# Kernel tuning notes

Measured on AMD Instinct MI355X. Metric: run time of the kernel, lower is better.

## Reference

```python
import jax, jax.numpy as jnp
import numpy as np

E = 128      # emb_size
VD = 128     # v_dim
NH = 4       # num_heads
WX = 7       # window_sizex
WY = 7       # window_sizey
B, HH, WW_ = 16, 112, 112


def setup_inputs() -> dict:
    key = jax.random.key(0)
    k0, k1, k2, k3 = jax.random.split(key, 4)
    return {
        "x": jax.random.normal(k0, (B, HH, WW_, E), jnp.float32),
        "v": jax.random.normal(k1, (B, HH, WW_, VD), jnp.float32),
        "Wqk": jax.random.normal(k2, (2 * E, E), jnp.float32) * 0.02,
        "bqk": jnp.zeros((2 * E,), jnp.float32),
        "pos_emb": jax.random.normal(k3, (2 * WX - 1, 2 * WY - 1), jnp.float32),
    }


def reference(x, v, Wqk, bqk, pos_emb):
    b, h, w, _ = x.shape
    e, ev = E // NH, VD // NH
    s = WX * WY
    Wh, Ww = h // WX, w // WY

    # qk projection: [b,h,w,2E] -> split as (c k) with c=E, k=2
    qk = (x @ Wqk.T + bqk).reshape(b, h, w, E, 2)

    # shifted roll: note original uses -window//2 = -4 (python floor div)
    qk = jnp.roll(qk, ((-WX) // 2, (-WY) // 2), axis=(1, 2))
    v = jnp.roll(v, ((-WX) // 2, (-WY) // 2), axis=(1, 2))

    # window partition; channel split is (e H): e outer, head inner
    qk = qk.reshape(b, Wh, WX, Ww, WY, e, NH, 2)
    qk = qk.transpose(0, 6, 1, 3, 2, 4, 5, 7).reshape(b, NH, Wh, Ww, s, e, 2)
    q, k_ = qk[..., 0], qk[..., 1]
    vw = v.reshape(b, Wh, WX, Ww, WY, ev, NH)
    vw = vw.transpose(0, 6, 1, 3, 2, 4, 5).reshape(b, NH, Wh, Ww, s, ev)

    scores = jnp.einsum('bhxyse,bhxyte->bhxyst', q, k_) / np.float32(np.sqrt(E / NH))

    # relative position bias lookup
    idx = np.indices((WX, WY)).transpose(1, 2, 0).reshape(s, 2)
    rel = idx[None, :, :] - idx[:, None, :] + np.array([WX - 1, WY - 1])
    scores = scores + pos_emb[rel[..., 0], rel[..., 1]]

    # shift masks (added to last window-row and last window-column)
    m = WX * (WY // 2)  # 21
    row_mask = np.zeros((s, s), np.float32)
    row_mask[-m:, :-m] = -np.inf
    row_mask[:-m, -m:] = -np.inf
    col_mask = row_mask.reshape(s // WX, WX, s // WY, WY).transpose(1, 0, 3, 2).reshape(s, s)
    scores = scores.at[:, :, -1, :].add(jnp.asarray(row_mask))
    scores = scores.at[:, :, :, -1].add(jnp.asarray(col_mask))

    attn = jax.nn.softmax(scores, axis=-1)
    out = jnp.einsum('bhxyst,bhxyte->bhxyse', attn, vw)

    # merge windows back: b H Wh Ww (w1 w2) e -> b (Wh w1) (Ww w2) (e H)
    out = out.reshape(b, NH, Wh, Ww, WX, WY, ev)
    out = out.transpose(0, 2, 4, 3, 5, 6, 1).reshape(b, h, w, VD)

    # un-roll: original uses +window//2 = +3 (asymmetric w.r.t. the -4 roll, kept faithful)
    out = jnp.roll(out, (WX // 2, WY // 2), axis=(1, 2))
    return out
```

## Files before the change

### kernel.cpp

```cpp
#include <hip/hip_runtime.h>
#include <hip/hip_bf16.h>
#include <math.h>

#define NH_ 4
#define S_  49
#define B_  16
#define H_  112
#define W_  112
#define WT  16

typedef __attribute__((ext_vector_type(8))) short short8;
typedef __attribute__((ext_vector_type(4))) float f32x4;

__device__ __forceinline__ unsigned short f2bf(float f) {
  union { __hip_bfloat16 h; unsigned short u; } c;
  c.h = __float2bfloat16(f);
  return c.u;
}
__device__ __forceinline__ short8 cvt8(float4 a, float4 b) {
  union { short8 s; unsigned short u[8]; } r;
  r.u[0] = f2bf(a.x); r.u[1] = f2bf(a.y); r.u[2] = f2bf(a.z); r.u[3] = f2bf(a.w);
  r.u[4] = f2bf(b.x); r.u[5] = f2bf(b.y); r.u[6] = f2bf(b.z); r.u[7] = f2bf(b.w);
  return r.s;
}

__global__ void wprep(const float* __restrict__ Wqk, unsigned short* __restrict__ Wb) {
  int oi = (blockIdx.x * 256 + threadIdx.x) * 4;
  int np = oi >> 7;
  int k  = oi & 127;
  int h = np >> 6, c = np & 63;
  int orig = 8 * (c >> 1) + 2 * h + (c & 1);
  float4 w = *(const float4*)(Wqk + orig * 128 + k);
  ushort4 o; o.x = f2bf(w.x); o.y = f2bf(w.y); o.z = f2bf(w.z); o.w = f2bf(w.w);
  *(ushort4*)(Wb + oi) = o;
}

#define PSTR   4112
#define SM_VT  32896
#define SM_POS 51328
#define SM_TOT 52004

__global__ __launch_bounds__(256, 3) void swin_fused(
    const float* __restrict__ x, const float* __restrict__ v,
    const float* __restrict__ bqk, const float* __restrict__ pos,
    const unsigned short* __restrict__ Wb, float* __restrict__ out)
{
  __shared__ __align__(16) char smem[SM_TOT];
  float* posl = (float*)(smem + SM_POS);

  const int tid  = threadIdx.x;
  const int lane = tid & 63;
  const int g    = lane >> 4, l15 = lane & 15;
  const int wv   = tid >> 6;
  const int blk  = blockIdx.x;
  const int ww   = blk % WT, wh = (blk / WT) % WT, b = blk / (WT * WT);

  if (tid < 169) posl[tid] = pos[tid];

  float bq[4];
  #pragma unroll
  for (int q = 0; q < 4; ++q)
    bq[q] = bqk[64 * q + 8 * (l15 >> 1) + 2 * wv + (l15 & 1)];

  float4 vS[8];
  #pragma unroll
  for (int it = 0; it < 2; ++it) {
    const int idx = tid + it * 256;
    const int e = idx & 31, p4 = idx >> 5;
    #pragma unroll
    for (int j = 0; j < 4; ++j) {
      const int p = p4 * 4 + j;
      float4 vv = {0.f, 0.f, 0.f, 0.f};
      if (p < S_) {
        const int px = p / 7, py = p % 7;
        const int gi = (wh * 7 + px + 4) % H_;
        const int gj = (ww * 7 + py + 4) % W_;
        vv = ((const float4*)(v + (((size_t)b * H_ + gi) * W_ + gj) * 128))[e];
      }
      vS[it * 4 + j] = vv;
    }
  }

  short8 af[4][4];
  #pragma unroll
  for (int mt = 0; mt < 4; ++mt) {
    const int prow = 16 * mt + l15;
    const int pc = prow < S_ ? prow : S_ - 1;
    const int px = pc / 7, py = pc % 7;
    const int gi = (wh * 7 + px + 4) % H_;
    const int gj = (ww * 7 + py + 4) % W_;
    const float* xrow = x + (((size_t)b * H_ + gi) * W_ + gj) * 128;
    #pragma unroll
    for (int kk = 0; kk < 4; ++kk) {
      float4 a0 = *(const float4*)(xrow + kk * 32 + g * 8);
      float4 a1 = *(const float4*)(xrow + kk * 32 + g * 8 + 4);
      af[mt][kk] = cvt8(a0, a1);
    }
  }

  #pragma unroll
  for (int it = 0; it < 2; ++it) {
    const int idx = tid + it * 256;
    const int e = idx & 31, p4 = idx >> 5;
    const int kbase = 32 * (p4 >> 3) + 8 * (p4 & 3) + 4 * ((p4 >> 2) & 1);
    union { ushort4 v4; unsigned short u[4]; } hv[4];
    #pragma unroll
    for (int j = 0; j < 4; ++j) {
      float4 vv = vS[it * 4 + j];
      hv[0].u[j] = f2bf(vv.x); hv[1].u[j] = f2bf(vv.y);
      hv[2].u[j] = f2bf(vv.z); hv[3].u[j] = f2bf(vv.w);
    }
    #pragma unroll
    for (int h = 0; h < 4; ++h)
      *(ushort4*)(smem + SM_VT + h * 4608 + e * 144 + kbase * 2) = hv[h].v4;
  }

  {
    char* plane0 = smem + (wv * 2) * PSTR;
    #pragma unroll
    for (int q = 0; q < 4; ++q) {
      const int nb = (wv * 64 + q * 16 + l15) * 128;
      short8 bfr[4];
      #pragma unroll
      for (int kk = 0; kk < 4; ++kk)
        bfr[kk] = *(const short8*)(Wb + nb + kk * 32 + g * 8);
      const float bias = bq[q];
      char* plane = plane0 + (l15 & 1) * PSTR;
      const int eoff = (q * 8 + (l15 >> 1)) * 2;
      #pragma unroll
      for (int mt = 0; mt < 4; ++mt) {
        f32x4 acc = {0.f, 0.f, 0.f, 0.f};
        #pragma unroll
        for (int kk = 0; kk < 4; ++kk)
          acc = __builtin_amdgcn_mfma_f32_16x16x32_bf16(af[mt][kk], bfr[kk], acc, 0, 0, 0);
        const int mbase = 16 * mt + 4 * g;
        #pragma unroll
        for (int r = 0; r < 4; ++r)
          *(unsigned short*)(plane + (mbase + r) * 64 + eoff) = f2bf(acc[r] + bias);
      }
    }
  }

  const bool maskR = (wh == WT - 1), maskC = (ww == WT - 1);
  const char* qpl = smem + (wv * 2 + 0) * PSTR;
  const char* kpl = smem + (wv * 2 + 1) * PSTR;
  short8 qf[4], kf[4];
  #pragma unroll
  for (int t4 = 0; t4 < 4; ++t4) {
    qf[t4] = *(const short8*)(qpl + (16 * t4 + l15) * 64 + g * 16);
    kf[t4] = *(const short8*)(kpl + (16 * t4 + l15) * 64 + g * 16);
  }

  f32x4 st[4][4];
  #pragma unroll
  for (int nt = 0; nt < 4; ++nt)
    #pragma unroll
    for (int mt = 0; mt < 4; ++mt) {
      f32x4 z = {0.f, 0.f, 0.f, 0.f};
      st[nt][mt] = __builtin_amdgcn_mfma_f32_16x16x32_bf16(kf[nt], qf[mt], z, 0, 0, 0);
    }

  int tix[4][4]; bool txg[4][4], tyg[4][4], tvl[4][4];
  #pragma unroll
  for (int nt = 0; nt < 4; ++nt)
    #pragma unroll
    for (int r = 0; r < 4; ++r) {
      const int t = 16 * nt + 4 * g + r;
      const int tx = t / 7, ty = t - 7 * tx;
      tix[nt][r] = tx * 13 + ty;
      txg[nt][r] = (tx >= 4); tyg[nt][r] = (ty >= 4);
      tvl[nt][r] = (t < S_);
    }

  if (maskR || maskC) {
    #pragma unroll
    for (int mt = 0; mt < 4; ++mt) {
      const int m = 16 * mt + l15;
      const int mc = m < S_ ? m : S_ - 1;
      const int px = mc / 7, py = mc - 7 * px;
      const bool pxg = (px >= 4), pyg = (py >= 4);
      #pragma unroll
      for (int nt = 0; nt < 4; ++nt)
        #pragma unroll
        for (int r = 0; r < 4; ++r) {
          if ((maskR && (pxg != txg[nt][r])) || (maskC && (pyg != tyg[nt][r])))
            st[nt][mt][r] = -INFINITY;
        }
    }
  }

  __syncthreads();

  const float scale = 0.17677669529663687f;
  short8 pvb[4][2];
  #pragma unroll
  for (int mt = 0; mt < 4; ++mt) {
    const int m = 16 * mt + l15;
    const int mc = m < S_ ? m : S_ - 1;
    const int px = mc / 7, py = mc - 7 * px;
    const int pofs = 84 - px * 13 - py;
    union { short8 s8; unsigned short h[8]; } pk[2];
    #pragma unroll
    for (int nt = 0; nt < 4; ++nt)
      #pragma unroll
      for (int r = 0; r < 4; ++r) {
        float s = st[nt][mt][r] * scale + posl[tix[nt][r] + pofs];
        float e = tvl[nt][r] ? __expf(s) : 0.f;
        pk[nt >> 1].h[(nt & 1) * 4 + r] = f2bf(e);
      }
    pvb[mt][0] = pk[0].s8;
    pvb[mt][1] = pk[1].s8;
  }

  f32x4 o_[2][4], d_[4];
  #pragma unroll
  for (int mt = 0; mt < 4; ++mt) {
    o_[0][mt] = (f32x4){0.f, 0.f, 0.f, 0.f};
    o_[1][mt] = (f32x4){0.f, 0.f, 0.f, 0.f};
    d_[mt]    = (f32x4){0.f, 0.f, 0.f, 0.f};
  }
  {
    const char* Vb = smem + SM_VT + wv * 4608;
    union { short8 s8; unsigned short h[8]; } one;
    #pragma unroll
    for (int j = 0; j < 8; ++j) one.h[j] = 0x3F80;
    #pragma unroll
    for (int ks = 0; ks < 2; ++ks) {
      short8 va[2];
      #pragma unroll
      for (int et = 0; et < 2; ++et)
        va[et] = *(const short8*)(Vb + (16 * et + l15) * 144 + ks * 64 + g * 16);
      #pragma unroll
      for (int mt = 0; mt < 4; ++mt) {
        o_[0][mt] = __builtin_amdgcn_mfma_f32_16x16x32_bf16(va[0], pvb[mt][ks], o_[0][mt], 0, 0, 0);
        o_[1][mt] = __builtin_amdgcn_mfma_f32_16x16x32_bf16(va[1], pvb[mt][ks], o_[1][mt], 0, 0, 0);
        d_[mt]    = __builtin_amdgcn_mfma_f32_16x16x32_bf16(one.s8, pvb[mt][ks], d_[mt], 0, 0, 0);
      }
    }
  }

  float (*outb)[132] = (float (*)[132])smem;
  #pragma unroll
  for (int mt = 0; mt < 4; ++mt) {
    const int m = 16 * mt + l15;
    if (m < S_) {
      const float inv = 1.f / d_[mt][0];
      #pragma unroll
      for (int et = 0; et < 2; ++et)
        #pragma unroll
        for (int r = 0; r < 4; ++r)
          outb[m][(16 * et + 4 * g + r) * 4 + wv] = o_[et][mt][r] * inv;
    }
  }
  __syncthreads();

  for (int idx = tid; idx < S_ * 32; idx += 256) {
    const int pp = idx >> 5, c4 = idx & 31;
    const int ppx = pp / 7, ppy = pp % 7;
    const int fi = (wh * 7 + ppx + 3) % H_;
    const int fj = (ww * 7 + ppy + 3) % W_;
    float4 val = *(const float4*)&outb[pp][c4 * 4];
    ((float4*)(out + (((size_t)b * H_ + fi) * W_ + fj) * 128))[c4] = val;
  }
}

extern "C" void kernel_launch(void* const* d_in, const int* in_sizes, int n_in,
                              void* d_out, int out_size, void* d_ws, size_t ws_size,
                              hipStream_t stream) {
  const float* x   = (const float*)d_in[0];
  const float* v   = (const float*)d_in[1];
  const float* Wqk = (const float*)d_in[2];
  const float* bqk = (const float*)d_in[3];
  const float* pos = (const float*)d_in[4];
  float* out = (float*)d_out;
  unsigned short* Wb = (unsigned short*)d_ws;

  hipLaunchKernelGGL(wprep, dim3(32), dim3(256), 0, stream, Wqk, Wb);
  hipLaunchKernelGGL(swin_fused, dim3(B_ * WT * WT), dim3(256), 0, stream,
                     x, v, bqk, pos, Wb, out);
}
```

Before: 110.5 us.

## Load V directly into MFMA register fragments, drop LDS staging, raise occupancy

V values are now gathered per lane straight from global memory as scalar floats, converted to bf16, and packed into MFMA B-operand fragments in registers. This removes the transposed LDS staging buffer for V and its stores and loads. Shared memory use drops from about 52KB to 33.5KB, and launch bounds go from 3 to 4 blocks per SM for more occupancy. In exchange, global loads become scalar and strided (one float per lane per element) instead of float4 and coalesced, and register pressure rises under the tighter launch bound.

```diff
diff --git a/kernel.cpp b/kernel.cpp
--- a/kernel.cpp
+++ b/kernel.cpp
@@ -36,11 +36,10 @@
 }
 
 #define PSTR   4112
-#define SM_VT  32896
-#define SM_POS 51328
-#define SM_TOT 52004
-
-__global__ __launch_bounds__(256, 3) void swin_fused(
+#define SM_POS 32896
+#define SM_TOT 33572
+
+__global__ __launch_bounds__(256, 4) void swin_fused(
     const float* __restrict__ x, const float* __restrict__ v,
     const float* __restrict__ bqk, const float* __restrict__ pos,
     const unsigned short* __restrict__ Wb, float* __restrict__ out)
@@ -62,23 +61,36 @@
   for (int q = 0; q < 4; ++q)
     bq[q] = bqk[64 * q + 8 * (l15 >> 1) + 2 * wv + (l15 & 1)];
 
-  float4 vS[8];
-  #pragma unroll
-  for (int it = 0; it < 2; ++it) {
-    const int idx = tid + it * 256;
-    const int e = idx & 31, p4 = idx >> 5;
-    #pragma unroll
-    for (int j = 0; j < 4; ++j) {
-      const int p = p4 * 4 + j;
-      float4 vv = {0.f, 0.f, 0.f, 0.f};
-      if (p < S_) {
-        const int px = p / 7, py = p % 7;
+  short8 vfr[2][2];
+  {
+    int voff[16]; bool vok[16];
+    #pragma unroll
+    for (int u = 0; u < 4; ++u)
+      #pragma unroll
+      for (int jr = 0; jr < 4; ++jr) {
+        const int t = 16 * u + 4 * g + jr;
+        const bool ok = (t < S_);
+        const int tc = ok ? t : 0;
+        const int px = tc / 7, py = tc - 7 * px;
         const int gi = (wh * 7 + px + 4) % H_;
         const int gj = (ww * 7 + py + 4) % W_;
-        vv = ((const float4*)(v + (((size_t)b * H_ + gi) * W_ + gj) * 128))[e];
-      }
-      vS[it * 4 + j] = vv;
-    }
+        voff[u * 4 + jr] = (gi * W_ + gj) * 128 + 4 * l15 + wv;
+        vok[u * 4 + jr] = ok;
+      }
+    const float* vb_ = v + (size_t)b * H_ * W_ * 128;
+    #pragma unroll
+    for (int et = 0; et < 2; ++et)
+      #pragma unroll
+      for (int ks = 0; ks < 2; ++ks) {
+        union { short8 s8; unsigned short h[8]; } pku;
+        #pragma unroll
+        for (int j = 0; j < 8; ++j) {
+          const int i16 = (2 * ks + (j >> 2)) * 4 + (j & 3);
+          float val = vok[i16] ? vb_[voff[i16] + et * 64] : 0.f;
+          pku.h[j] = f2bf(val);
+        }
+        vfr[et][ks] = pku.s8;
+      }
   }
 
   short8 af[4][4];
@@ -98,23 +110,6 @@
     }
   }
 
-  #pragma unroll
-  for (int it = 0; it < 2; ++it) {
-    const int idx = tid + it * 256;
-    const int e = idx & 31, p4 = idx >> 5;
-    const int kbase = 32 * (p4 >> 3) + 8 * (p4 & 3) + 4 * ((p4 >> 2) & 1);
-    union { ushort4 v4; unsigned short u[4]; } hv[4];
-    #pragma unroll
-    for (int j = 0; j < 4; ++j) {
-      float4 vv = vS[it * 4 + j];
-      hv[0].u[j] = f2bf(vv.x); hv[1].u[j] = f2bf(vv.y);
-      hv[2].u[j] = f2bf(vv.z); hv[3].u[j] = f2bf(vv.w);
-    }
-    #pragma unroll
-    for (int h = 0; h < 4; ++h)
-      *(ushort4*)(smem + SM_VT + h * 4608 + e * 144 + kbase * 2) = hv[h].v4;
-  }
-
   {
     char* plane0 = smem + (wv * 2) * PSTR;
     #pragma unroll
@@ -220,21 +215,16 @@
     d_[mt]    = (f32x4){0.f, 0.f, 0.f, 0.f};
   }
   {
-    const char* Vb = smem + SM_VT + wv * 4608;
     union { short8 s8; unsigned short h[8]; } one;
     #pragma unroll
     for (int j = 0; j < 8; ++j) one.h[j] = 0x3F80;
     #pragma unroll
     for (int ks = 0; ks < 2; ++ks) {
-      short8 va[2];
-      #pragma unroll
-      for (int et = 0; et < 2; ++et)
-        va[et] = *(const short8*)(Vb + (16 * et + l15) * 144 + ks * 64 + g * 16);
       #pragma unroll
       for (int mt = 0; mt < 4; ++mt) {
-        o_[0][mt] = __builtin_amdgcn_mfma_f32_16x16x32_bf16(va[0], pvb[mt][ks], o_[0][mt], 0, 0, 0);
-        o_[1][mt] = __builtin_amdgcn_mfma_f32_16x16x32_bf16(va[1], pvb[mt][ks], o_[1][mt], 0, 0, 0);
-        d_[mt]    = __builtin_amdgcn_mfma_f32_16x16x32_bf16(one.s8, pvb[mt][ks], d_[mt], 0, 0, 0);
+        o_[0][mt] = __builtin_amdgcn_mfma_f32_16x16x32_bf16(vfr[0][ks], pvb[mt][ks], o_[0][mt], 0, 0, 0);
+        o_[1][mt] = __builtin_amdgcn_mfma_f32_16x16x32_bf16(vfr[1][ks], pvb[mt][ks], o_[1][mt], 0, 0, 0);
+        d_[mt]    = __builtin_amdgcn_mfma_f32_16x16x32_bf16(one.s8,    pvb[mt][ks], d_[mt],    0, 0, 0);
       }
     }
   }
```

Result: slower. 196.1 us (+77.5%).
